# Kernel optimization log

Hardware: AMD Instinct MI355X
Metric: run time of the kernel (lower is better)

## Reference

```python
import jax, jax.numpy as jnp
import numpy as np

T, B, D = 512, 16, 128   # cur_seq, batch, d_input
H = 8                    # n_heads
DH = D                   # d_head_inner = d_input in TemporalTX
P = 512                  # prev_seq = hgcn_rollout_len


def setup_inputs() -> dict:
    key = jax.random.key(0)
    ks = jax.random.split(key, 8)
    inp = {
        "inputs": jax.random.normal(ks[0], (T, B, D), jnp.float32),
        "memory": jax.random.normal(ks[1], (2, P, B, D), jnp.float32),  # n_layers+1 = 2
        "w_kv": jax.random.normal(ks[2], (2 * H * DH, D), jnp.float32) * 0.02,
        "w_q": jax.random.normal(ks[3], (H * DH, D), jnp.float32) * 0.02,
        "w_p": jax.random.normal(ks[4], (H * DH, D), jnp.float32) * 0.02,
        "w_out": jax.random.normal(ks[5], (D, H * DH), jnp.float32) * 0.02,
        "u": jax.random.normal(ks[6], (H, DH), jnp.float32) * 0.02,
        "v": jax.random.normal(ks[7], (H, DH), jnp.float32) * 0.02,
    }
    return inp


def _rel_shift(x):
    # x: [I, J, B, H] -> Transformer-XL relative shift
    I, J, b, h = x.shape
    zp = jnp.zeros((I, 1, b, h), x.dtype)
    return jnp.concatenate([zp, x], axis=1).reshape(J + 1, I, b, h)[1:].reshape(I, J, b, h)


def _pos_embs(J, d):
    # positions counting down: J-1 ... 0
    pos = jnp.arange(J - 1, -1, -1, dtype=jnp.float32)
    inv_freq = 1.0 / (10000.0 ** (jnp.arange(0.0, d, 2.0) / d))
    sin_inp = pos[:, None] * inv_freq[None, :]          # [J, d/2]
    return jnp.concatenate([jnp.sin(sin_inp), jnp.cos(sin_inp)], axis=-1)  # [J, d]


def _attention(x, mem, pe, w_kv, w_q, w_p, w_out, u, v, mask):
    cs, bs, _ = x.shape
    J = cs + mem.shape[0]
    xm = jnp.concatenate([mem, x], axis=0)              # [J, B, D]
    kv = jnp.einsum('jbe,fe->jbf', xm, w_kv)            # [J, B, 2*H*DH]
    k, vv = jnp.split(kv, 2, axis=-1)
    k = k.reshape(J, bs, H, DH)
    vv = vv.reshape(J, bs, H, DH)
    q = jnp.einsum('ibe,fe->ibf', x, w_q).reshape(cs, bs, H, DH)
    content = jnp.einsum('ibhd,jbhd->ijbh', q + u, k)   # [I, J, B, H]
    p = jnp.einsum('je,fe->jf', pe, w_p).reshape(J, H, DH)
    position = jnp.einsum('ibhd,jhd->ijbh', q + v, p)
    position = _rel_shift(position)
    attn = content + position
    attn = jnp.where(mask[:, :, None, None], -jnp.inf, attn)
    scale = 1.0 / (DH ** 0.5)
    attn = jax.nn.softmax(attn * scale, axis=1)
    out = jnp.einsum('ijbh,jbhd->ibhd', attn, vv).reshape(cs, bs, H * DH)
    return jnp.einsum('ibf,ef->ibe', out, w_out)        # [I, B, D]


def reference(inputs, memory, w_kv, w_q, w_p, w_out, u, v):
    cs, bs = inputs.shape[:2]
    mem = list(memory)                                   # unbind along layer dim
    ps = mem[0].shape[0]
    J = cs + ps
    mask = jnp.triu(jnp.ones((cs, J), bool), k=1 + ps)   # [cs, J]
    pe = _pos_embs(J, D)                                 # [J, D]
    layer_out = _attention(inputs, mem[0], pe, w_kv, w_q, w_p, w_out, u, v, mask)
    hidden = [inputs, layer_out]
    # update_memory: keep last ps entries of cat(mem, hidden), detached
    new_mem = []
    end = ps + cs
    beg = max(0, end - ps)
    for m, h in zip(mem, hidden):
        cat = jnp.concatenate([m, h], axis=0)
        new_mem.append(jax.lax.stop_gradient(cat[beg:end]))
    return layer_out, jnp.stack(new_mem)
```

## Files before the change

### kernel.cpp

```cpp
#include <hip/hip_runtime.h>


typedef short s16x8 __attribute__((ext_vector_type(8)));
typedef float f32x4 __attribute__((ext_vector_type(4)));

#define MFMA(a, b, c) __builtin_amdgcn_mfma_f32_16x16x32_bf16((a), (b), (c), 0, 0, 0)
#define LDS_FENCE() asm volatile("s_waitcnt lgkmcnt(0)" ::: "memory")

__device__ __forceinline__ unsigned short f2b(float f) {
  unsigned int x = __builtin_bit_cast(unsigned int, f);
  x += 0x7fffu + ((x >> 16) & 1u);
  return (unsigned short)(x >> 16);
}
__device__ __forceinline__ s16x8 ldg8(const unsigned short* p) {
  return *(const s16x8*)p;
}
__device__ __forceinline__ s16x8 ldf8(const float* p) {
  float4 u = ((const float4*)p)[0];
  float4 v = ((const float4*)p)[1];
  s16x8 r;
  r[0] = (short)f2b(u.x); r[1] = (short)f2b(u.y);
  r[2] = (short)f2b(u.z); r[3] = (short)f2b(u.w);
  r[4] = (short)f2b(v.x); r[5] = (short)f2b(v.y);
  r[6] = (short)f2b(v.z); r[7] = (short)f2b(v.w);
  return r;
}
__device__ __forceinline__ void gl2lds(const unsigned short* g, unsigned short* l) {
  __builtin_amdgcn_global_load_lds(
      (const __attribute__((address_space(1))) unsigned int*)(g),
      (__attribute__((address_space(3))) unsigned int*)(l), 16, 0, 0);
}

__global__ __launch_bounds__(256, 2) void k_prep(
    const float* __restrict__ wkv, const float* __restrict__ wq,
    const float* __restrict__ wp, const float* __restrict__ wout,
    unsigned short* __restrict__ wkv_b, unsigned short* __restrict__ wq_b,
    unsigned short* __restrict__ wp_b, unsigned short* __restrict__ wout_b) {
  int id = blockIdx.x * 256 + threadIdx.x;
  const float* src;
  unsigned short* dst;
  int off;
  if (id < 32768) { src = wkv; dst = wkv_b; off = id; }
  else if (id < 49152) { src = wq; dst = wq_b; off = id - 32768; }
  else if (id < 65536) { src = wp; dst = wp_b; off = id - 49152; }
  else { src = wout; dst = wout_b; off = id - 65536; }
  ((s16x8*)dst)[off] = ldf8(src + off * 8);
}

__global__ __launch_bounds__(256, 2) void k_gemm_kv(
    const float* __restrict__ x, const float* __restrict__ mem,
    const unsigned short* __restrict__ wkv_b,
    unsigned short* __restrict__ Kk, unsigned short* __restrict__ Vt) {
  __shared__ float tbuf[4][16][128];
  const int lane = threadIdx.x & 63;
  const int w = threadIdx.x >> 6;
  const int ncg = (blockIdx.x & 3) * 4;
  const int b = (blockIdx.x >> 2) & 15;
  const int jb = (blockIdx.x >> 6) * 128 + w * 32;
  const int l15 = lane & 15, l4 = lane >> 4;

  s16x8 A[2][4];
#pragma unroll
  for (int g = 0; g < 2; ++g) {
    int jr = jb + g * 16 + l15;
    const float* arow =
        (jr < 512 ? mem + (jr * 16 + b) * 128 : x + ((jr - 512) * 16 + b) * 128) + l4 * 8;
    A[g][0] = ldf8(arow); A[g][1] = ldf8(arow + 32);
    A[g][2] = ldf8(arow + 64); A[g][3] = ldf8(arow + 96);
  }

  for (int q = 0; q < 4; ++q) {
    const int nc = ncg + q;
    f32x4 acc[2][8] = {};
#pragma unroll
    for (int fc = 0; fc < 8; ++fc) {
      const unsigned short* brow = wkv_b + (nc * 128 + fc * 16 + l15) * 128 + l4 * 8;
      s16x8 b0 = ldg8(brow), b1 = ldg8(brow + 32), b2 = ldg8(brow + 64), b3 = ldg8(brow + 96);
#pragma unroll
      for (int g = 0; g < 2; ++g) {
        acc[g][fc] = MFMA(A[g][0], b0, acc[g][fc]);
        acc[g][fc] = MFMA(A[g][1], b1, acc[g][fc]);
        acc[g][fc] = MFMA(A[g][2], b2, acc[g][fc]);
        acc[g][fc] = MFMA(A[g][3], b3, acc[g][fc]);
      }
    }

    if (nc < 8) {
#pragma unroll
      for (int g = 0; g < 2; ++g)
#pragma unroll
        for (int fc = 0; fc < 8; ++fc)
#pragma unroll
          for (int r = 0; r < 4; ++r) {
            int j = jb + g * 16 + l4 * 4 + r;
            Kk[((b * 8 + nc) * 1024 + j) * 128 + fc * 16 + l15] = f2b(acc[g][fc][r]);
          }
    } else {
      const int h = nc - 8;
#pragma unroll
      for (int g = 0; g < 2; ++g) {
        LDS_FENCE();
#pragma unroll
        for (int fc = 0; fc < 8; ++fc)
#pragma unroll
          for (int r = 0; r < 4; ++r) tbuf[w][l4 * 4 + r][fc * 16 + l15] = acc[g][fc][r];
        LDS_FENCE();
#pragma unroll
        for (int half = 0; half < 2; ++half) {
          int dd = half * 64 + lane;
          unsigned int wd[8];
#pragma unroll
          for (int pw = 0; pw < 8; ++pw) {
            unsigned int lo = f2b(tbuf[w][2 * pw][dd]);
            unsigned int hi = f2b(tbuf[w][2 * pw + 1][dd]);
            wd[pw] = lo | (hi << 16);
          }
          unsigned short* dst = Vt + ((b * 8 + h) * 128 + dd) * 1024 + jb + g * 16;
          ((uint4*)dst)[0] = make_uint4(wd[0], wd[1], wd[2], wd[3]);
          ((uint4*)dst)[1] = make_uint4(wd[4], wd[5], wd[6], wd[7]);
        }
      }
    }
  }
}

__global__ __launch_bounds__(256, 2) void k_gemm_p(
    const unsigned short* __restrict__ wp_b, unsigned short* __restrict__ Pp) {
  const int lane = threadIdx.x & 63;
  const int w = threadIdx.x >> 6;
  const int nc = blockIdx.x & 7;
  const int c0 = ((blockIdx.x >> 3) * 4 + w) * 16;
  const int l15 = lane & 15, l4 = lane >> 4;

  const float pos = (float)(1023 - (c0 + l15));
  s16x8 a[4];
#pragma unroll
  for (int ks = 0; ks < 4; ++ks)
#pragma unroll
    for (int jj = 0; jj < 8; ++jj) {
      int e = ks * 32 + l4 * 8 + jj;
      int t = e & 63;
      float ang = pos * exp2f(-0.20762050593046014f * (float)t);
      float val = (e < 64) ? sinf(ang) : cosf(ang);
      a[ks][jj] = (short)f2b(val);
    }

  f32x4 acc[8] = {};
#pragma unroll
  for (int fc = 0; fc < 8; ++fc) {
    const unsigned short* brow = wp_b + (nc * 128 + fc * 16 + l15) * 128 + l4 * 8;
    acc[fc] = MFMA(a[0], ldg8(brow), acc[fc]);
    acc[fc] = MFMA(a[1], ldg8(brow + 32), acc[fc]);
    acc[fc] = MFMA(a[2], ldg8(brow + 64), acc[fc]);
    acc[fc] = MFMA(a[3], ldg8(brow + 96), acc[fc]);
  }
#pragma unroll
  for (int fc = 0; fc < 8; ++fc)
#pragma unroll
    for (int r = 0; r < 4; ++r)
      Pp[(nc * 1024 + c0 + l4 * 4 + r) * 128 + fc * 16 + l15] = f2b(acc[fc][r]);
}

__global__ __launch_bounds__(256, 2) void k_flash(
    const float* __restrict__ x, const unsigned short* __restrict__ wq_b,
    const unsigned short* __restrict__ Kk, const unsigned short* __restrict__ Vt,
    const unsigned short* __restrict__ Pp,
    const float* __restrict__ uu, const float* __restrict__ vv,
    unsigned short* __restrict__ OA) {
  __shared__ __align__(16) unsigned short L[37376];
  unsigned short* LK = L;
  unsigned short* LV = L + 8192;
  unsigned short* LP = L + 16384;
  unsigned short* PB = L + 32768;

  const int lane = threadIdx.x & 63;
  const int w = threadIdx.x >> 6;
  const int bh = blockIdx.x & 127;
  const int igw = 7 - (blockIdx.x >> 7);
  const int iw = igw * 64 + w * 16;
  const int b = bh >> 3, h = bh & 7;
  const int l15 = lane & 15, l4 = lane >> 4;
  const float CSCALE = 0.08838834764831845f * 1.4426950408889634f;

  const unsigned short* K_b = Kk + bh * (1024 * 128);
  const unsigned short* V_b = Vt + bh * (128 * 1024);
  const unsigned short* P_h = Pp + h * (1024 * 128);

  s16x8 qu[4], qv[4];
  {
    const float* arow = x + ((iw + l15) * 16 + b) * 128 + l4 * 8;
    s16x8 a0 = ldf8(arow), a1 = ldf8(arow + 32), a2 = ldf8(arow + 64), a3 = ldf8(arow + 96);
    f32x4 qd[8] = {};
#pragma unroll
    for (int fc = 0; fc < 8; ++fc) {
      const unsigned short* brow = wq_b + (h * 128 + fc * 16 + l15) * 128 + l4 * 8;
      qd[fc] = MFMA(a0, ldg8(brow), qd[fc]);
      qd[fc] = MFMA(a1, ldg8(brow + 32), qd[fc]);
      qd[fc] = MFMA(a2, ldg8(brow + 64), qd[fc]);
      qd[fc] = MFMA(a3, ldg8(brow + 96), qd[fc]);
    }
    unsigned short* qs = LP + w * 2176;
#pragma unroll
    for (int fc = 0; fc < 8; ++fc) {
      float ud = uu[h * 128 + fc * 16 + l15];
#pragma unroll
      for (int r = 0; r < 4; ++r) qs[(l4 * 4 + r) * 136 + fc * 16 + l15] = f2b(qd[fc][r] + ud);
    }
    LDS_FENCE();
#pragma unroll
    for (int ks = 0; ks < 4; ++ks)
      qu[ks] = *(const s16x8*)&qs[l15 * 136 + ks * 32 + l4 * 8];
    LDS_FENCE();
#pragma unroll
    for (int fc = 0; fc < 8; ++fc) {
      float vd = vv[h * 128 + fc * 16 + l15];
#pragma unroll
      for (int r = 0; r < 4; ++r) qs[(l4 * 4 + r) * 136 + fc * 16 + l15] = f2b(qd[fc][r] + vd);
    }
    LDS_FENCE();
#pragma unroll
    for (int ks = 0; ks < 4; ++ks)
      qv[ks] = *(const s16x8*)&qs[l15 * 136 + ks * 32 + l4 * 8];
  }
  __syncthreads();

  f32x4 O[8] = {};
  float rs[4] = {0.f, 0.f, 0.f, 0.f};

  const int tmax = igw + 9;
  for (int t = 0; t < tmax; ++t) {
    const int j0 = t * 64;
    const int cbase = j0 - igw * 64 + 448;

#pragma unroll
    for (int q = 0; q < 4; ++q) {
      int c = w * 4 + q, s = c & 7;
      gl2lds(K_b + (j0 + (lane ^ s)) * 128 + c * 8, LK + c * 512);
    }
#pragma unroll
    for (int q = 0; q < 4; ++q) {
      int m = w * 4 + q, c = m >> 1, hh = m & 1;
      gl2lds(V_b + (hh * 64 + (lane ^ c)) * 1024 + j0 + c * 8,
             LV + (c * 128 + hh * 64) * 8);
    }
#pragma unroll
    for (int q = 0; q < 8; ++q) {
      int m = w * 8 + q, c = m >> 1, hh = m & 1, s = c & 7;
      int grow = cbase + hh * 64 + (lane ^ s);
      grow = (grow > 1023) ? 1023 : grow;
      gl2lds(P_h + grow * 128 + c * 8, LP + (c * 128 + hh * 64) * 8);
    }
    __syncthreads();

    f32x4 sc[4];
#pragma unroll
    for (int fc = 0; fc < 4; ++fc) {
      f32x4 t4 = {};
#pragma unroll
      for (int ks = 0; ks < 4; ++ks) {
        int c = ks * 4 + l4, s = c & 7;
        t4 = MFMA(qu[ks], *(const s16x8*)&LK[(c * 64 + ((fc * 16 + l15) ^ s)) * 8], t4);
      }
      sc[fc] = t4;
    }
    f32x4 sp[5];
#pragma unroll
    for (int pc = 0; pc < 5; ++pc) {
      f32x4 t4 = {};
      int prow = 48 - w * 16 + pc * 16 + l15;
#pragma unroll
      for (int ks = 0; ks < 4; ++ks) {
        int c = ks * 4 + l4, s = c & 7;
        t4 = MFMA(qv[ks], *(const s16x8*)&LP[(c * 128 + (prow ^ s)) * 8], t4);
      }
      sp[pc] = t4;
    }

    unsigned short* pb = PB + w * 1152;
#pragma unroll
    for (int fc = 0; fc < 4; ++fc)
#pragma unroll
      for (int r = 0; r < 4; ++r) {
        int li = l4 * 4 + r;
        int jj = fc * 16 + l15;
        int cc = jj - li + 15;
        int src = (lane & 48) | (cc & 15);
        float g0 = __shfl(sp[fc][r], src, 64);
        float g1 = __shfl(sp[fc + 1][r], src, 64);
        float pv = ((cc >> 4) == fc) ? g0 : g1;
        float logit = (sc[fc][r] + pv) * CSCALE - 12.0f;
        if (j0 + jj > iw + li + 512) logit = -72.0f;
        float p = exp2f(logit);
        rs[r] += p;
        pb[li * 72 + jj] = f2b(p);
      }

    s16x8 pa0 = *(const s16x8*)&pb[l15 * 72 + l4 * 8];
    s16x8 pa1 = *(const s16x8*)&pb[l15 * 72 + 32 + l4 * 8];
#pragma unroll
    for (int fd = 0; fd < 8; ++fd) {
      int row = fd * 16 + l15;
      int c0v = l4, c1v = 4 + l4;
      O[fd] = MFMA(pa0, *(const s16x8*)&LV[(c0v * 128 + (row ^ c0v)) * 8], O[fd]);
      O[fd] = MFMA(pa1, *(const s16x8*)&LV[(c1v * 128 + (row ^ c1v)) * 8], O[fd]);
    }
    __syncthreads();
  }

  float lrow[4];
#pragma unroll
  for (int r = 0; r < 4; ++r) {
    float s = rs[r];
#pragma unroll
    for (int off = 1; off < 16; off <<= 1) s += __shfl_xor(s, off, 64);
    lrow[r] = s;
  }
#pragma unroll
  for (int fd = 0; fd < 8; ++fd)
#pragma unroll
    for (int r = 0; r < 4; ++r) {
      int li = l4 * 4 + r;
      float o = O[fd][r] / lrow[r];
      OA[((iw + li) * 16 + b) * 1024 + h * 128 + fd * 16 + l15] = f2b(o);
    }
}

__global__ __launch_bounds__(256, 2) void k_out(
    const unsigned short* __restrict__ OA, const unsigned short* __restrict__ wout_b,
    const float* __restrict__ x, float* __restrict__ out) {
  const int lane = threadIdx.x & 63;
  const int w = threadIdx.x >> 6;
  const int half = blockIdx.x & 1;
  const int rt = (blockIdx.x >> 1) * 4 + w;
  const int l15 = lane & 15, l4 = lane >> 4;

  f32x4 acc[4] = {};
  const unsigned short* arow = OA + (rt * 16 + l15) * 1024 + l4 * 8;
#pragma unroll 4
  for (int ks = 0; ks < 32; ++ks) {
    s16x8 a = ldg8(arow + ks * 32);
#pragma unroll
    for (int fc = 0; fc < 4; ++fc) {
      const unsigned short* brow =
          wout_b + (half * 64 + fc * 16 + l15) * 1024 + ks * 32 + l4 * 8;
      acc[fc] = MFMA(a, ldg8(brow), acc[fc]);
    }
  }
#pragma unroll
  for (int fc = 0; fc < 4; ++fc)
#pragma unroll
    for (int r = 0; r < 4; ++r) {
      int rg = rt * 16 + l4 * 4 + r;
      int e = half * 64 + fc * 16 + l15;
      float v = acc[fc][r];
      out[rg * 128 + e] = v;
      out[2097152 + rg * 128 + e] = v;
    }
  const float4* src = (const float4*)(x + rt * 2048 + half * 1024);
  float4* dst = (float4*)(out + 1048576 + rt * 2048 + half * 1024);
  dst[lane] = src[lane];
  dst[64 + lane] = src[64 + lane];
  dst[128 + lane] = src[128 + lane];
  dst[192 + lane] = src[192 + lane];
}

extern "C" void kernel_launch(void* const* d_in, const int* in_sizes, int n_in,
                              void* d_out, int out_size, void* d_ws, size_t ws_size,
                              hipStream_t stream) {
  (void)in_sizes; (void)n_in; (void)out_size; (void)ws_size;
  const float* x    = (const float*)d_in[0];
  const float* mem  = (const float*)d_in[1];
  const float* wkv  = (const float*)d_in[2];
  const float* wq   = (const float*)d_in[3];
  const float* wp   = (const float*)d_in[4];
  const float* wout = (const float*)d_in[5];
  const float* uu   = (const float*)d_in[6];
  const float* vv   = (const float*)d_in[7];
  float* out = (float*)d_out;
  unsigned short* ws = (unsigned short*)d_ws;

  unsigned short* Kk     = ws;
  unsigned short* Vt     = ws + 16777216;
  unsigned short* Pp     = ws + 33554432;
  unsigned short* OA     = ws + 34603008;
  unsigned short* wkv_b  = ws + 42991616;
  unsigned short* wq_b   = ws + 43253760;
  unsigned short* wp_b   = ws + 43384832;
  unsigned short* wout_b = ws + 43515904;

  k_prep<<<320, 256, 0, stream>>>(wkv, wq, wp, wout, wkv_b, wq_b, wp_b, wout_b);
  k_gemm_kv<<<512, 256, 0, stream>>>(x, mem, wkv_b, Kk, Vt);
  k_gemm_p<<<128, 256, 0, stream>>>(wp_b, Pp);
  k_flash<<<1024, 256, 0, stream>>>(x, wq_b, Kk, Vt, Pp, uu, vv, OA);
  k_out<<<256, 256, 0, stream>>>(OA, wout_b, x, out);
}
```

Before: 312.7 us.

## Store K/V/P tiles in MFMA fragment order and reuse P tiles via ring buffer

Global-to-LDS loads now write K, V and positional tiles directly in per-lane MFMA fragment order, so the compute loops read LDS with a simple lane*8 offset instead of XOR-swizzled addressing. Positional embedding rows are kept in an 8-slot ring buffer: the first iteration loads 128 rows and each later one fetches only the 64 new rows, reusing the overlap between consecutive tiles. This cuts P global traffic per iteration roughly in half and simplifies address math. It relies on the ring-slot indexing staying consistent across iterations, and the fragment layout may cause LDS bank conflicts on the gather writes.

```diff
diff --git a/kernel.cpp b/kernel.cpp
--- a/kernel.cpp
+++ b/kernel.cpp
@@ -180,6 +180,7 @@
   const int iw = igw * 64 + w * 16;
   const int b = bh >> 3, h = bh & 7;
   const int l15 = lane & 15, l4 = lane >> 4;
+  const int cb4 = 28 - igw * 4;
   const float CSCALE = 0.08838834764831845f * 1.4426950408889634f;
 
   const unsigned short* K_b = Kk + bh * (1024 * 128);
@@ -230,25 +231,33 @@
   const int tmax = igw + 9;
   for (int t = 0; t < tmax; ++t) {
     const int j0 = t * 64;
-    const int cbase = j0 - igw * 64 + 448;
-
+
+#pragma unroll
+    for (int q = 0; q < 4; ++q)
+      gl2lds(K_b + (j0 + w * 16 + l15) * 128 + q * 32 + l4 * 8, LK + (w * 4 + q) * 512);
 #pragma unroll
     for (int q = 0; q < 4; ++q) {
-      int c = w * 4 + q, s = c & 7;
-      gl2lds(K_b + (j0 + (lane ^ s)) * 128 + c * 8, LK + c * 512);
-    }
-#pragma unroll
-    for (int q = 0; q < 4; ++q) {
-      int m = w * 4 + q, c = m >> 1, hh = m & 1;
-      gl2lds(V_b + (hh * 64 + (lane ^ c)) * 1024 + j0 + c * 8,
-             LV + (c * 128 + hh * 64) * 8);
-    }
-#pragma unroll
-    for (int q = 0; q < 8; ++q) {
-      int m = w * 8 + q, c = m >> 1, hh = m & 1, s = c & 7;
-      int grow = cbase + hh * 64 + (lane ^ s);
-      grow = (grow > 1023) ? 1023 : grow;
-      gl2lds(P_h + grow * 128 + c * 8, LP + (c * 128 + hh * 64) * 8);
+      int m = w * 4 + q, fd = m >> 1, ks = m & 1;
+      gl2lds(V_b + (fd * 16 + l15) * 1024 + j0 + ks * 32 + l4 * 8, LV + m * 512);
+    }
+    if (t == 0) {
+#pragma unroll
+      for (int q = 0; q < 8; ++q) {
+        int m = w * 8 + q, rc = m >> 2, ks = m & 3;
+        int gchunk = cb4 + rc, slot = gchunk & 7;
+        int grow = gchunk * 16 + l15;
+        grow = (grow > 1023) ? 1023 : grow;
+        gl2lds(P_h + grow * 128 + ks * 32 + l4 * 8, LP + (slot * 4 + ks) * 512);
+      }
+    } else {
+#pragma unroll
+      for (int q = 0; q < 4; ++q) {
+        int m = w * 4 + q, gcq = m >> 2, ks = m & 3;
+        int gchunk = cb4 + 4 * t + 4 + gcq, slot = gchunk & 7;
+        int grow = gchunk * 16 + l15;
+        grow = (grow > 1023) ? 1023 : grow;
+        gl2lds(P_h + grow * 128 + ks * 32 + l4 * 8, LP + (slot * 4 + ks) * 512);
+      }
     }
     __syncthreads();
 
@@ -257,22 +266,18 @@
     for (int fc = 0; fc < 4; ++fc) {
       f32x4 t4 = {};
 #pragma unroll
-      for (int ks = 0; ks < 4; ++ks) {
-        int c = ks * 4 + l4, s = c & 7;
-        t4 = MFMA(qu[ks], *(const s16x8*)&LK[(c * 64 + ((fc * 16 + l15) ^ s)) * 8], t4);
-      }
+      for (int ks = 0; ks < 4; ++ks)
+        t4 = MFMA(qu[ks], *(const s16x8*)&LK[(fc * 4 + ks) * 512 + lane * 8], t4);
       sc[fc] = t4;
     }
     f32x4 sp[5];
 #pragma unroll
     for (int pc = 0; pc < 5; ++pc) {
       f32x4 t4 = {};
-      int prow = 48 - w * 16 + pc * 16 + l15;
-#pragma unroll
-      for (int ks = 0; ks < 4; ++ks) {
-        int c = ks * 4 + l4, s = c & 7;
-        t4 = MFMA(qv[ks], *(const s16x8*)&LP[(c * 128 + (prow ^ s)) * 8], t4);
-      }
+      int slot = (cb4 + 4 * t + 3 - w + pc) & 7;
+#pragma unroll
+      for (int ks = 0; ks < 4; ++ks)
+        t4 = MFMA(qv[ks], *(const s16x8*)&LP[(slot * 4 + ks) * 512 + lane * 8], t4);
       sp[pc] = t4;
     }
 
@@ -299,10 +304,8 @@
     s16x8 pa1 = *(const s16x8*)&pb[l15 * 72 + 32 + l4 * 8];
 #pragma unroll
     for (int fd = 0; fd < 8; ++fd) {
-      int row = fd * 16 + l15;
-      int c0v = l4, c1v = 4 + l4;
-      O[fd] = MFMA(pa0, *(const s16x8*)&LV[(c0v * 128 + (row ^ c0v)) * 8], O[fd]);
-      O[fd] = MFMA(pa1, *(const s16x8*)&LV[(c1v * 128 + (row ^ c1v)) * 8], O[fd]);
+      O[fd] = MFMA(pa0, *(const s16x8*)&LV[(fd * 2) * 512 + lane * 8], O[fd]);
+      O[fd] = MFMA(pa1, *(const s16x8*)&LV[(fd * 2 + 1) * 512 + lane * 8], O[fd]);
     }
     __syncthreads();
   }
```

New measurement: 283.9 us. -9.2%, faster.
